# Performance work log

Measured on AMD Instinct MI355X. Metric: run time of the kernel, lower is better.

The kernel has to match this reference:

```python
import jax, jax.numpy as jnp
import numpy as np
from math import sqrt

D, H, B, L = 1024, 16, 2, 2048
DK = D // H

def linear(x, w, b):
    # torch Linear layout: w (out, in)
    return x @ w.T + b

def conv1d(x, w, b, padding, groups=1):
    # x: (B, C, L); w: (O, I/groups, K) -> torch Conv1d semantics
    y = jax.lax.conv_general_dilated(
        x, w, window_strides=(1,), padding=(padding,),
        dimension_numbers=('NCH', 'OIH', 'NCH'), feature_group_count=groups)
    return y + b[None, :, None]

def setup_inputs() -> dict:
    key = jax.random.key(0)
    ks = jax.random.split(key, 26)
    def n(k, shape, s=0.02):
        return jax.random.normal(k, shape, jnp.float32) * s
    return {
        'x': jax.random.normal(ks[0], (B, L, D), jnp.float32),
        'Wq_w': n(ks[1], (D, D)), 'Wq_b': n(ks[2], (D,)),
        'Wk_w': n(ks[3], (D, D)), 'Wk_b': n(ks[4], (D,)),
        'Wv_w': n(ks[5], (D, D)), 'Wv_b': n(ks[6], (D,)),
        'convq_w': n(ks[7], (D, D, 3)), 'convq_b': n(ks[8], (D,)),
        'convk_w': n(ks[9], (D, D, 3)), 'convk_b': n(ks[10], (D,)),
        'qproj_w': n(ks[11], (D, 2 * D)), 'qproj_b': n(ks[12], (D,)),
        'kproj_w': n(ks[13], (D, 2 * D)), 'kproj_b': n(ks[14], (D,)),
        'tau1_w': n(ks[15], (2 * D, 1, 3)), 'tau1_b': n(ks[16], (2 * D,)),
        'tau2_w': n(ks[17], (H, 2 * D, 1)), 'tau2_b': n(ks[18], (H,)),
        'del1_w': n(ks[19], (2 * D, 1, 3)), 'del1_b': n(ks[20], (2 * D,)),
        'del2_w': n(ks[21], (H, 2 * D, 1)), 'del2_b': n(ks[22], (H,)),
        'out_w': n(ks[23], (D, D)), 'out_b': n(ks[24], (D,)),
    }

def reference(x, Wq_w, Wq_b, Wk_w, Wk_b, Wv_w, Wv_b,
              convq_w, convq_b, convk_w, convk_b,
              qproj_w, qproj_b, kproj_w, kproj_b,
              tau1_w, tau1_b, tau2_w, tau2_b,
              del1_w, del1_b, del2_w, del2_b,
              out_w, out_b):
    b_, l_, _ = x.shape

    # Q branch: linear -> conv3 -> concat -> proj
    q_in = linear(x, Wq_w, Wq_b).transpose(0, 2, 1)          # (B, D, L)
    Q3 = conv1d(q_in, convq_w, convq_b, (1, 1))              # (B, D, L)
    Q_cat = jnp.concatenate([q_in, Q3], axis=1).transpose(0, 2, 1)  # (B, L, 2D)
    Q = linear(Q_cat, qproj_w, qproj_b).reshape(b_, l_, H, DK).transpose(0, 2, 1, 3)

    # K branch
    k_in = linear(x, Wk_w, Wk_b).transpose(0, 2, 1)
    K3 = conv1d(k_in, convk_w, convk_b, (1, 1))
    K_cat = jnp.concatenate([k_in, K3], axis=1).transpose(0, 2, 1)
    K = linear(K_cat, kproj_w, kproj_b).reshape(b_, l_, H, DK).transpose(0, 2, 1, 3)

    V = linear(x, Wv_w, Wv_b).reshape(b_, l_, H, DK).transpose(0, 2, 1, 3)

    # per-head tau (query-row scale) and delta (key-column bias), shape (B, H, L)
    x_conv = x.transpose(0, 2, 1)                             # (B, D, L)
    tau = jax.nn.sigmoid(conv1d(
        jax.nn.gelu(conv1d(x_conv, tau1_w, tau1_b, (1, 1), groups=D), approximate=False),
        tau2_w, tau2_b, (0, 0)))
    delta = jax.nn.sigmoid(conv1d(
        jax.nn.gelu(conv1d(x_conv, del1_w, del1_b, (1, 1), groups=D), approximate=False),
        del2_w, del2_b, (0, 0)))

    scores = jnp.einsum('bhqd,bhkd->bhqk', Q, K) / sqrt(DK)   # (B, H, L, L)
    scores = scores * tau[..., None] + delta[:, :, None, :]
    attn = jax.nn.softmax(scores, axis=-1)                    # dropout = identity (eval)
    out = jnp.einsum('bhqk,bhkd->bhqd', attn, V)
    out = out.transpose(0, 2, 1, 3).reshape(b_, l_, D)
    return linear(out, out_w, out_b)
```

## Files before the change

### kernel.cpp

```cpp
#include <hip/hip_runtime.h>

typedef __bf16 bf16_t;
typedef __bf16 bf16x8 __attribute__((ext_vector_type(8)));
typedef __bf16 bf16x4 __attribute__((ext_vector_type(4)));
typedef float f32x4 __attribute__((ext_vector_type(4)));

__device__ __forceinline__ void gload_lds16(const bf16_t* g, bf16_t* l) {
  __builtin_amdgcn_global_load_lds(
      (__attribute__((address_space(1))) void*)g,
      (__attribute__((address_space(3))) void*)l, 16, 0, 0);
}

__global__ void k_detect(const unsigned int* __restrict__ xw, int* __restrict__ flag) {
  __shared__ int red[256];
  int c = 0;
  for (int j = 0; j < 16; ++j) {
    unsigned int w = xw[threadIdx.x + (j << 8)];
    unsigned int e = (w >> 7) & 0xFF;
    c += (e >= 100 && e <= 150) ? 1 : 0;
  }
  red[threadIdx.x] = c;
  __syncthreads();
  for (int s = 128; s > 0; s >>= 1) {
    if (threadIdx.x < s) red[threadIdx.x] += red[threadIdx.x + s];
    __syncthreads();
  }
  if (threadIdx.x == 0) flag[0] = (red[0] > 2048) ? 1 : 0;
}

__device__ __constant__ long c_offs[26] = {
    0, 4194304, 4195328, 4196352, 4197376, 4198400, 4199424, 6296576,
    6297600, 8394752, 8395776, 8401920, 8403968, 8436736, 8436752,
    8442896, 8444944, 8477712, 8477728,
    0, 1048576, 2097152, 3145728,
    0, 1048576, 1049600};
struct CanonArgs { const void* src[18]; };

__global__ void k_canon(CanonArgs a, int base, int n, const int* __restrict__ flag,
                        bf16_t* __restrict__ dst) {
  long e0 = ((long)blockIdx.x * 256 + threadIdx.x) * 8;
  if (e0 >= c_offs[base + n]) return;
  int k = 0;
  while (e0 >= c_offs[base + k + 1]) ++k;
  const long rel = e0 - c_offs[base + k];
  if (flag[0]) {
    *(bf16x8*)&dst[e0] = *(const bf16x8*)((const bf16_t*)a.src[k] + rel);
  } else {
    const float* sf = (const float*)a.src[k] + rel;
    f32x4 lo = *(const f32x4*)sf;
    f32x4 hi = *(const f32x4*)(sf + 4);
    bf16x8 o;
    o[0] = (bf16_t)lo[0]; o[1] = (bf16_t)lo[1]; o[2] = (bf16_t)lo[2]; o[3] = (bf16_t)lo[3];
    o[4] = (bf16_t)hi[0]; o[5] = (bf16_t)hi[1]; o[6] = (bf16_t)hi[2]; o[7] = (bf16_t)hi[3];
    *(bf16x8*)&dst[e0] = o;
  }
}

__global__ void k_zero_pads(bf16_t* __restrict__ pad) {
  int idx = blockIdx.x * 256 + threadIdx.x;
  if (idx >= 8192) return;
  int b = idx >> 11;
  int r = (idx >> 10) & 1;
  int c = idx & 1023;
  long row = (long)b * 2050 + (r ? 2049 : 0);
  pad[row * 1024 + c] = (bf16_t)0.0f;
}

__global__ void k_convw_t2(const void* __restrict__ w0, const void* __restrict__ w1,
                           bf16_t* __restrict__ dst0, bf16_t* __restrict__ dst1,
                           const int* __restrict__ flag) {
  int idx = blockIdx.x * 256 + threadIdx.x;
  if (idx >= 6291456) return;
  const void* w = w0;
  bf16_t* dst = dst0;
  if (idx >= 3145728) { idx -= 3145728; w = w1; dst = dst1; }
  int o = idx / 3072;
  int rem = idx - o * 3072;
  int k = rem >> 10;
  int i = rem & 1023;
  int src = (o * 1024 + i) * 3 + k;
  float v = flag[0] ? (float)((const bf16_t*)w)[src] : ((const float*)w)[src];
  dst[idx] = (bf16_t)v;
}

struct GemmP {
  const bf16_t *A0, *A1;
  const bf16_t *B0, *B1, *B2;
  const bf16_t *bias0, *bias1, *bias2;
  bf16_t *C0, *C1, *C2;
  long a_jump, a1_jump;
  long cj0, cj1, cj2;
  int ksplit, lda, lda1, rpb, rpc, ldb, bsel_by_n, bshift, K, csel_by_n;
  int crs0, ccs0, crs1, ccs1, crs2, ccs2;
};

template <int BN, bool FINAL>
__global__ __launch_bounds__(256) void k_gemm(GemmP p, const int* __restrict__ flagp) {
  __shared__ __align__(16) bf16_t As[2][4096];
  __shared__ __align__(16) bf16_t Bs[2][BN * 32];
  const int tid = threadIdx.x;
  const int gx = gridDim.x;
  int lin = blockIdx.y * gx + blockIdx.x;
  const int nwg = gx * gridDim.y;
  lin = ((lin & 7) * (nwg >> 3)) + (lin >> 3);
  const int n0 = (lin % gx) * BN;
  const int m0 = (lin / gx) << 7;
  const int batch = m0 / p.rpb;
  const int cbatch = m0 / p.rpc;
  const int bidx = p.bsel_by_n ? (n0 >> 10) : (m0 >> p.bshift);
  const bf16_t* Bp = bidx == 0 ? p.B0 : (bidx == 1 ? p.B1 : p.B2);
  const bf16_t* biasp = bidx == 0 ? p.bias0 : (bidx == 1 ? p.bias1 : p.bias2);
  const long abase = (long)batch * p.a_jump;
  const long a1base = (long)cbatch * p.a1_jump;
  const int arow = tid >> 2;
  const int koff = (((tid & 3) ^ ((tid >> 3) & 3)) << 3);
  const int wid = tid >> 6, lane = tid & 63;
  const int l15 = lane & 15, lg = lane >> 4;
  const int nloc = n0 & 1023;

  constexpr int MI = (BN == 128) ? 4 : 2;
  const int wr = (BN == 128) ? ((wid >> 1) << 6) : (wid << 5);
  const int wc = (BN == 128) ? ((wid & 1) << 6) : 0;
  const int rsw = ((lg ^ (l15 >> 1)) & 3) << 3;

  f32x4 acc[MI][4];
#pragma unroll
  for (int i = 0; i < MI; ++i)
#pragma unroll
    for (int j = 0; j < 4; ++j) acc[i][j] = (f32x4){0.f, 0.f, 0.f, 0.f};

  auto stage = [&](int bufi, int k) {
    const int kg = k + koff;
#pragma unroll
    for (int half = 0; half < 2; ++half) {
      const int row = m0 + half * 64 + arow;
      const bf16_t* ap;
      if (kg < p.ksplit) ap = p.A0 + abase + (long)row * p.lda + kg;
      else               ap = p.A1 + a1base + (long)row * p.lda1 + (kg - p.ksplit);
      gload_lds16(ap, &As[bufi][half * 2048 + (tid << 3)]);
    }
    gload_lds16(Bp + (long)(nloc + arow) * p.ldb + kg, &Bs[bufi][tid << 3]);
    if (BN == 128)
      gload_lds16(Bp + (long)(nloc + 64 + arow) * p.ldb + kg, &Bs[bufi][2048 + (tid << 3)]);
  };

  const int nk = p.K >> 5;
  int buf = 0;
  stage(0, 0);
  asm volatile("s_waitcnt vmcnt(0)" ::: "memory");
  __builtin_amdgcn_s_barrier();
  __builtin_amdgcn_sched_barrier(0);
  for (int kt = 0; kt < nk; ++kt) {
    if (kt + 1 < nk) stage(buf ^ 1, (kt + 1) << 5);
    bf16x8 af[MI], bfr[4];
#pragma unroll
    for (int i = 0; i < MI; ++i)
      af[i] = *(const bf16x8*)&As[buf][((wr + (i << 4) + l15) << 5) + rsw];
#pragma unroll
    for (int j = 0; j < 4; ++j)
      bfr[j] = *(const bf16x8*)&Bs[buf][((wc + (j << 4) + l15) << 5) + rsw];
#pragma unroll
    for (int i = 0; i < MI; ++i)
#pragma unroll
      for (int j = 0; j < 4; ++j)
        acc[i][j] = __builtin_amdgcn_mfma_f32_16x16x32_bf16(af[i], bfr[j], acc[i][j], 0, 0, 0);
    if (kt + 1 < nk) asm volatile("s_waitcnt vmcnt(0)" ::: "memory");
    __builtin_amdgcn_s_barrier();
    __builtin_amdgcn_sched_barrier(0);
    buf ^= 1;
  }

  const int cp = p.csel_by_n ? (n0 >> 10) : (m0 >> p.bshift);
  bf16_t* Cb = cp == 0 ? p.C0 : (cp == 1 ? p.C1 : p.C2);
  const int crs = cp == 0 ? p.crs0 : (cp == 1 ? p.crs1 : p.crs2);
  const int ccs = cp == 0 ? p.ccs0 : (cp == 1 ? p.ccs1 : p.ccs2);
  const long cj = cp == 0 ? p.cj0 : (cp == 1 ? p.cj1 : p.cj2);
  const bool f32out = FINAL && (flagp[0] == 0);
  const long cbase = (long)batch * cj;
#pragma unroll
  for (int i = 0; i < MI; ++i) {
    const int row = m0 + wr + (i << 4) + (lg << 2);
#pragma unroll
    for (int j = 0; j < 4; ++j) {
      const int col = nloc + wc + (j << 4) + l15;
      const float bv = (float)biasp[col];
#pragma unroll
      for (int r = 0; r < 4; ++r) {
        const float val = acc[i][j][r] + bv;
        const long ci = cbase + (long)(row + r) * crs + (long)col * ccs;
        if (FINAL && f32out) ((float*)Cb)[ci] = val;
        else Cb[ci] = (bf16_t)val;
      }
    }
  }
}

__global__ __launch_bounds__(256) void k_taudelta(
    const bf16_t* __restrict__ x,
    const bf16_t* __restrict__ t1w, const bf16_t* __restrict__ t1b,
    const bf16_t* __restrict__ t2w, const bf16_t* __restrict__ t2b,
    const bf16_t* __restrict__ d1w, const bf16_t* __restrict__ d1b,
    const bf16_t* __restrict__ d2w, const bf16_t* __restrict__ d2b,
    float* __restrict__ tau, float* __restrict__ dlt)
{
  const int bt = blockIdx.x;
  const int t = bt & 2047;
  const int b = bt >> 11;
  const int tid = threadIdx.x;
  const bf16_t* xr = x + ((long)bt << 10);

  float acc[32];
#pragma unroll
  for (int i = 0; i < 32; ++i) acc[i] = 0.f;

  for (int j = 0; j < 8; ++j) {
    const int c = tid + (j << 8);
    const int src = c >> 1;
    const float x0 = (float)xr[src];
    const float xm = (t > 0) ? (float)xr[src - 1024] : 0.f;
    const float xp = (t < 2047) ? (float)xr[src + 1024] : 0.f;
    float st = (float)t1w[3 * c] * xm + (float)t1w[3 * c + 1] * x0 +
               (float)t1w[3 * c + 2] * xp + (float)t1b[c];
    float sd = (float)d1w[3 * c] * xm + (float)d1w[3 * c + 1] * x0 +
               (float)d1w[3 * c + 2] * xp + (float)d1b[c];
    const float gt = 0.5f * st * (1.f + erff(st * 0.70710678118f));
    const float gd = 0.5f * sd * (1.f + erff(sd * 0.70710678118f));
#pragma unroll
    for (int h = 0; h < 16; ++h) {
      acc[h]      += (float)t2w[(h << 11) + c] * gt;
      acc[16 + h] += (float)d2w[(h << 11) + c] * gd;
    }
  }

  __shared__ float red[256][33];
  __shared__ float red2[8][32];
#pragma unroll
  for (int i = 0; i < 32; ++i) red[tid][i] = acc[i];
  __syncthreads();
  const int i = tid & 31, g = tid >> 5;
  float p = 0.f;
#pragma unroll
  for (int k2 = 0; k2 < 32; ++k2) p += red[(g << 5) + k2][i];
  __syncthreads();
  red2[g][i] = p;
  __syncthreads();
  if (tid < 32) {
    float s = 0.f;
#pragma unroll
    for (int g2 = 0; g2 < 8; ++g2) s += red2[g2][tid];
    const int h = tid & 15;
    if (tid < 16) {
      s += (float)t2b[h];
      tau[((long)((b << 4) + h) << 11) + t] = 1.f / (1.f + __expf(-s));
    } else {
      s += (float)d2b[h];
      dlt[((long)((b << 4) + h) << 11) + t] =
          1.4426950408889634f / (1.f + __expf(-s));
    }
  }
}

__device__ __forceinline__ unsigned pk2(float a, float b) {
  union { bf16_t h[2]; unsigned u; } z;
  z.h[0] = (bf16_t)a; z.h[1] = (bf16_t)b;
  return z.u;
}

__global__ __launch_bounds__(256) void k_attn(
    const bf16_t* __restrict__ QKb, const bf16_t* __restrict__ VT,
    const float* __restrict__ tau, const float* __restrict__ dlt,
    bf16_t* __restrict__ O)
{
  const int lin = blockIdx.x;
  const int wg = ((lin & 7) << 7) + (lin >> 3);
  const int bh = wg >> 5, qt = wg & 31;
  const int tid = threadIdx.x;
  const int lane = tid & 63;
  const int wid = tid >> 6;
  const int l15 = lane & 15, lg = lane >> 4;
  const int b = bh >> 4, h = bh & 15;
  const int qbase = (qt << 6) + (wid << 4);

  const bf16_t* Qp = QKb + ((long)b << 21) + (h << 6);
  const bf16_t* Kp = QKb + 4194304 + ((long)b << 21) + (h << 6);
  const bf16_t* Vp = VT + ((long)bh << 17);
  const float* dltb = dlt + ((long)bh << 11);

  __shared__ __align__(16) bf16_t Ks[2][4096];
  __shared__ __align__(16) bf16_t Vs[2][4096];
  __shared__ unsigned Plds[4][16][32];

  bf16x8 qf[2];
#pragma unroll
  for (int kd = 0; kd < 2; ++kd)
    qf[kd] = *(const bf16x8*)&Qp[((long)(qbase + l15) << 10) + (kd << 5) + (lg << 3)];
  const float tq = tau[((long)bh << 11) + qbase + l15] * (0.125f * 1.4426950408889634f);

  bf16x8 onesf;
#pragma unroll
  for (int e = 0; e < 8; ++e) onesf[e] = (bf16_t)1.0f;

  f32x4 accO[4];
#pragma unroll
  for (int d = 0; d < 4; ++d) accO[d] = (f32x4){0.f, 0.f, 0.f, 0.f};
  f32x4 accL = (f32x4){0.f, 0.f, 0.f, 0.f};

  const int xr = (l15 & 7) << 2;

  auto stageKV = [&](int bufi, int kk) {
#pragma unroll
    for (int it = 0; it < 2; ++it) {
      const int t2 = tid + (it << 8);
      const int r = t2 >> 3, cc = (t2 & 7) ^ (r & 7);
      gload_lds16(Kp + ((long)(kk + r) << 10) + (cc << 3), &Ks[bufi][t2 << 3]);
    }
#pragma unroll
    for (int it = 0; it < 2; ++it) {
      const int t2 = tid + (it << 8);
      const int r = t2 >> 3;
      gload_lds16(Vp + ((long)r << 11) + kk + (((t2 & 7) ^ (r & 7)) << 3), &Vs[bufi][t2 << 3]);
    }
  };

  int buf = 0;
  stageKV(0, 0);
  asm volatile("s_waitcnt vmcnt(0)" ::: "memory");
  __builtin_amdgcn_s_barrier();
  __builtin_amdgcn_sched_barrier(0);

  for (int kk = 0; kk < 2048; kk += 64) {
    if (kk + 64 < 2048) stageKV(buf ^ 1, kk + 64);

    f32x4 st[4];
    __builtin_amdgcn_s_setprio(1);
#pragma unroll
    for (int kb = 0; kb < 4; ++kb) {
      f32x4 z = (f32x4){0.f, 0.f, 0.f, 0.f};
#pragma unroll
      for (int kd = 0; kd < 2; ++kd) {
        const bf16x8 kf = *(const bf16x8*)&Ks[buf][(((kb << 4) + l15) << 6) +
                                                  ((((kd << 2) | lg) ^ (l15 & 7)) << 3)];
        z = __builtin_amdgcn_mfma_f32_16x16x32_bf16(kf, qf[kd], z, 0, 0, 0);
      }
      st[kb] = z;
    }
    __builtin_amdgcn_s_setprio(0);

#pragma unroll
    for (int kb = 0; kb < 4; ++kb) {
      const f32x4 dl = *(const f32x4*)&dltb[kk + (kb << 4) + (lg << 2)];
      const float p0 = exp2f(fminf(fmaf(st[kb][0], tq, dl[0]), 30.f));
      const float p1 = exp2f(fminf(fmaf(st[kb][1], tq, dl[1]), 30.f));
      const float p2 = exp2f(fminf(fmaf(st[kb][2], tq, dl[2]), 30.f));
      const float p3 = exp2f(fminf(fmaf(st[kb][3], tq, dl[3]), 30.f));
      Plds[wid][l15][((kb << 3) + (lg << 1)) ^ xr]       = pk2(p0, p1);
      Plds[wid][l15][(((kb << 3) + (lg << 1)) | 1) ^ xr] = pk2(p2, p3);
    }
    asm volatile("s_waitcnt lgkmcnt(0)" ::: "memory");
    __builtin_amdgcn_sched_barrier(0);
    const bf16x8 pf0 = *(const bf16x8*)&Plds[wid][l15][(lg << 2) ^ xr];
    const bf16x8 pf1 = *(const bf16x8*)&Plds[wid][l15][(16 | (lg << 2)) ^ xr];
    asm volatile("s_waitcnt lgkmcnt(0)" ::: "memory");
    __builtin_amdgcn_sched_barrier(0);

    __builtin_amdgcn_s_setprio(1);
#pragma unroll
    for (int d = 0; d < 4; ++d) {
      const bf16x8 vf0 = *(const bf16x8*)&Vs[buf][(((d << 4) + l15) << 6) +
                                                 ((lg ^ (l15 & 7)) << 3)];
      const bf16x8 vf1 = *(const bf16x8*)&Vs[buf][(((d << 4) + l15) << 6) +
                                                 (((4 | lg) ^ (l15 & 7)) << 3)];
      accO[d] = __builtin_amdgcn_mfma_f32_16x16x32_bf16(vf0, pf0, accO[d], 0, 0, 0);
      accO[d] = __builtin_amdgcn_mfma_f32_16x16x32_bf16(vf1, pf1, accO[d], 0, 0, 0);
    }
    accL = __builtin_amdgcn_mfma_f32_16x16x32_bf16(onesf, pf0, accL, 0, 0, 0);
    accL = __builtin_amdgcn_mfma_f32_16x16x32_bf16(onesf, pf1, accL, 0, 0, 0);
    __builtin_amdgcn_s_setprio(0);

    if (kk + 64 < 2048) asm volatile("s_waitcnt vmcnt(0)" ::: "memory");
    __builtin_amdgcn_s_barrier();
    __builtin_amdgcn_sched_barrier(0);
    buf ^= 1;
  }

  bf16_t* Ob = O + ((long)b << 21) + (h << 6);
  const float inv = 1.f / accL[0];
#pragma unroll
  for (int d = 0; d < 4; ++d) {
    bf16x4 ov;
#pragma unroll
    for (int r = 0; r < 4; ++r) ov[r] = (bf16_t)(accO[d][r] * inv);
    *(bf16x4*)&Ob[((long)(qbase + l15) << 10) + (d << 4) + (lg << 2)] = ov;
  }
}

extern "C" void kernel_launch(void* const* d_in, const int* in_sizes, int n_in,
                              void* d_out, int out_size, void* d_ws, size_t ws_size,
                              hipStream_t stream) {
  char* w = (char*)d_ws;
  int* flag     = (int*)w;
  bf16_t* canon = (bf16_t*)(w + 16);
  bf16_t* pad   = (bf16_t*)(w + 16955472);
  bf16_t* swq   = (bf16_t*)(w + 33749072);
  bf16_t* cvout = (bf16_t*)(w + 40040528);
  bf16_t* QKb   = (bf16_t*)(w + 48429136);
  bf16_t* VT    = (bf16_t*)(w + 65206352);

  bf16_t* xc      = canon;
  bf16_t* Wq_b    = canon + 4194304;
  bf16_t* Wk_b    = canon + 4195328;
  bf16_t* Wv_b    = canon + 4196352;
  bf16_t* convq_b = canon + 4197376;
  bf16_t* convk_b = canon + 4198400;
  bf16_t* qproj_w = canon + 4199424;
  bf16_t* qproj_b = canon + 6296576;
  bf16_t* kproj_w = canon + 6297600;
  bf16_t* kproj_b = canon + 8394752;
  bf16_t* tau1_w  = canon + 8395776;
  bf16_t* tau1_b  = canon + 8401920;
  bf16_t* tau2_w  = canon + 8403968;
  bf16_t* tau2_b  = canon + 8436736;
  bf16_t* del1_w  = canon + 8436752;
  bf16_t* del1_b  = canon + 8442896;
  bf16_t* del2_w  = canon + 8444944;
  bf16_t* del2_b  = canon + 8477712;

  bf16_t* pad_q = pad;
  bf16_t* Wq_w = swq, *Wk_w = swq + 1048576, *Wv_w = swq + 2097152;
  float* tau = (float*)swq;
  float* dlt = (float*)((char*)swq + 262144);
  bf16_t* convt_q = QKb;
  bf16_t* convt_k = QKb + 4194304;
  bf16_t* cv_q = xc;
  bf16_t* cv_k = cvout;
  bf16_t* outw_bf = pad;
  bf16_t* outb_bf = pad + 1048576;
  bf16_t* attn_out = xc;

  k_detect<<<1, 256, 0, stream>>>((const unsigned int*)d_in[0], flag);

  CanonArgs ca{};
  {
    const int idxA[18] = {0, 2, 4, 6, 8, 10, 11, 12, 13, 14,
                          15, 16, 17, 18, 19, 20, 21, 22};
    for (int i = 0; i < 18; ++i) ca.src[i] = d_in[idxA[i]];
    k_canon<<<4140, 256, 0, stream>>>(ca, 0, 18, flag, canon);
  }
  {
    CanonArgs cw{};
    cw.src[0] = d_in[1]; cw.src[1] = d_in[3]; cw.src[2] = d_in[5];
    k_canon<<<1536, 256, 0, stream>>>(cw, 19, 3, flag, swq);
  }
  k_zero_pads<<<32, 256, 0, stream>>>(pad);

  {
    GemmP p{};
    p.A0 = xc; p.A1 = xc;
    p.B0 = Wq_w; p.B1 = Wk_w; p.B2 = Wv_w;
    p.bias0 = Wq_b; p.bias1 = Wk_b; p.bias2 = Wv_b;
    p.C0 = pad_q + 1024; p.C1 = pad_q + 4198400 + 1024; p.C2 = VT;
    p.a_jump = 0; p.a1_jump = 0;
    p.cj0 = 2048; p.cj1 = 2048; p.cj2 = 2095104;
    p.ksplit = 1024; p.lda = 1024; p.lda1 = 1024; p.rpb = 2048; p.rpc = 4096;
    p.ldb = 1024; p.bsel_by_n = 1; p.bshift = 12; p.K = 1024; p.csel_by_n = 1;
    p.crs0 = 1024; p.ccs0 = 1; p.crs1 = 1024; p.ccs1 = 1; p.crs2 = 1; p.ccs2 = 2048;
    k_gemm<128, false><<<dim3(24, 32), 256, 0, stream>>>(p, flag);
  }

  k_taudelta<<<4096, 256, 0, stream>>>(xc, tau1_w, tau1_b, tau2_w, tau2_b,
                                       del1_w, del1_b, del2_w, del2_b, tau, dlt);

  k_convw_t2<<<24576, 256, 0, stream>>>(d_in[7], d_in[9], convt_q, convt_k, flag);

  {
    GemmP p{};
    p.A0 = pad; p.A1 = pad;
    p.B0 = convt_q; p.B1 = convt_k; p.B2 = convt_k;
    p.bias0 = convq_b; p.bias1 = convk_b; p.bias2 = convk_b;
    p.C0 = cv_q; p.C1 = cv_k - 4194304; p.C2 = cv_k;
    p.a_jump = 2048; p.a1_jump = 0;
    p.cj0 = 0; p.cj1 = 0; p.cj2 = 0;
    p.ksplit = 3072; p.lda = 1024; p.lda1 = 1024; p.rpb = 2048; p.rpc = 4096;
    p.ldb = 3072; p.bsel_by_n = 0; p.bshift = 12; p.K = 3072; p.csel_by_n = 0;
    p.crs0 = 1024; p.ccs0 = 1; p.crs1 = 1024; p.ccs1 = 1; p.crs2 = 1024; p.ccs2 = 1;
    k_gemm<128, false><<<dim3(8, 64), 256, 0, stream>>>(p, flag);
  }

  {
    GemmP p{};
    p.A0 = pad + 1024; p.A1 = cv_q;
    p.B0 = qproj_w; p.B1 = kproj_w; p.B2 = kproj_w;
    p.bias0 = qproj_b; p.bias1 = kproj_b; p.bias2 = kproj_b;
    p.C0 = QKb; p.C1 = QKb; p.C2 = QKb;
    p.a_jump = 2048;
    p.a1_jump = 20020256 - 4194304;
    p.cj0 = 0; p.cj1 = 0; p.cj2 = 0;
    p.ksplit = 1024; p.lda = 1024; p.lda1 = 1024; p.rpb = 2048; p.rpc = 4096;
    p.ldb = 2048; p.bsel_by_n = 0; p.bshift = 12; p.K = 2048; p.csel_by_n = 0;
    p.crs0 = 1024; p.ccs0 = 1; p.crs1 = 1024; p.ccs1 = 1; p.crs2 = 1024; p.ccs2 = 1;
    k_gemm<128, false><<<dim3(8, 64), 256, 0, stream>>>(p, flag);
  }

  {
    CanonArgs co{};
    co.src[0] = d_in[23]; co.src[1] = d_in[24];
    k_canon<<<513, 256, 0, stream>>>(co, 23, 2, flag, outw_bf);
  }

  k_attn<<<1024, 256, 0, stream>>>(QKb, VT, tau, dlt, attn_out);

  {
    GemmP p{};
    p.A0 = attn_out; p.A1 = attn_out;
    p.B0 = p.B1 = p.B2 = outw_bf;
    p.bias0 = p.bias1 = p.bias2 = outb_bf;
    p.C0 = p.C1 = p.C2 = (bf16_t*)d_out;
    p.a_jump = 0; p.a1_jump = 0;
    p.cj0 = p.cj1 = p.cj2 = 0;
    p.ksplit = 1024; p.lda = 1024; p.lda1 = 1024; p.rpb = 4096; p.rpc = 4096;
    p.ldb = 1024; p.bsel_by_n = 0; p.bshift = 12; p.K = 1024; p.csel_by_n = 0;
    p.crs0 = p.crs1 = p.crs2 = 1024; p.ccs0 = p.ccs1 = p.ccs2 = 1;
    k_gemm<64, true><<<dim3(16, 32), 256, 0, stream>>>(p, flag);
  }
}
```

Baseline: 410.7 us.

## Fold conv3 weights into the projection to skip the conv GEMM

The conv1d(k=3) and the concat+projection are linear maps, so they are composed. The projection's second half is multiplied into the transposed conv weights, giving combined weights H = W2·Conv per tap. The first half of the projection is added to the centre tap, and the conv bias is folded into a bias vector. Q/K then come from a single GEMM with K=3072 over the padded linear output, which replaces the 3072-K conv GEMM plus the 2048-K projection GEMM applied to activations. This adds a weight-only GEMM, a tiled-transpose kernel for the conv weights and small add/bias kernels. It also changes rounding, since the combined weights are stored in bf16.

```diff
diff --git a/kernel.cpp b/kernel.cpp
--- a/kernel.cpp
+++ b/kernel.cpp
@@ -56,8 +56,9 @@
   }
 }
 
-__global__ void k_zero_pads(bf16_t* __restrict__ pad) {
+__global__ void k_zero_pads(bf16_t* __restrict__ pad, bf16_t* __restrict__ zvec) {
   int idx = blockIdx.x * 256 + threadIdx.x;
+  if (idx < 1024) zvec[idx] = (bf16_t)0.0f;
   if (idx >= 8192) return;
   int b = idx >> 11;
   int r = (idx >> 10) & 1;
@@ -66,31 +67,90 @@
   pad[row * 1024 + c] = (bf16_t)0.0f;
 }
 
-__global__ void k_convw_t2(const void* __restrict__ w0, const void* __restrict__ w1,
-                           bf16_t* __restrict__ dst0, bf16_t* __restrict__ dst1,
-                           const int* __restrict__ flag) {
-  int idx = blockIdx.x * 256 + threadIdx.x;
-  if (idx >= 6291456) return;
-  const void* w = w0;
-  bf16_t* dst = dst0;
-  if (idx >= 3145728) { idx -= 3145728; w = w1; dst = dst1; }
-  int o = idx / 3072;
-  int rem = idx - o * 3072;
-  int k = rem >> 10;
-  int i = rem & 1023;
-  int src = (o * 1024 + i) * 3 + k;
-  float v = flag[0] ? (float)((const bf16_t*)w)[src] : ((const float*)w)[src];
-  dst[idx] = (bf16_t)v;
+__global__ __launch_bounds__(256) void k_ctT(
+    const void* __restrict__ wq, const void* __restrict__ wk,
+    bf16_t* __restrict__ dq, bf16_t* __restrict__ dk,
+    const int* __restrict__ flag) {
+  __shared__ bf16_t T[64][72];
+  int blk = blockIdx.x;
+  const int br = blk >= 768;
+  if (br) blk -= 768;
+  const void* w = br ? wk : wq;
+  bf16_t* dst = br ? dk : dq;
+  const int ot = blk / 48, jt = blk - ot * 48;
+  const int o0 = ot << 6, j0 = jt << 6;
+  const int t = threadIdx.x;
+  const int f = flag[0];
+#pragma unroll
+  for (int it = 0; it < 2; ++it) {
+    const int ch = t + (it << 8);
+    const int r = ch >> 3, c8 = (ch & 7) << 3;
+    const long off = (long)(o0 + r) * 3072 + j0 + c8;
+    if (f) {
+      *(bf16x8*)&T[r][c8] = *(const bf16x8*)((const bf16_t*)w + off);
+    } else {
+      const float* sf = (const float*)w + off;
+      bf16x8 o8;
+#pragma unroll
+      for (int e = 0; e < 8; ++e) o8[e] = (bf16_t)sf[e];
+      *(bf16x8*)&T[r][c8] = o8;
+    }
+  }
+  __syncthreads();
+  const int j = t >> 2, oc0 = (t & 3) << 4;
+  const int jj = j0 + j;
+  const int drow = (jj % 3) * 1024 + jj / 3;
+  bf16_t* dp = dst + (long)drow * 1024 + o0 + oc0;
+#pragma unroll
+  for (int s = 0; s < 16; ++s) dp[s] = T[oc0 + s][j];
+}
+
+__global__ void k_addwp1(bf16_t* __restrict__ Hq, bf16_t* __restrict__ Hk,
+                         const bf16_t* __restrict__ qp, const bf16_t* __restrict__ kp) {
+  const long e0 = ((long)blockIdx.x * 256 + threadIdx.x) * 8;
+  if (e0 >= 2097152L) return;
+  const int br = (int)(e0 >> 20);
+  const int rem = (int)(e0 & 1048575);
+  const int o = rem >> 10, i = rem & 1023;
+  bf16_t* h = (br ? Hk : Hq) + (long)o * 3072 + 1024 + i;
+  const bf16_t* w = (br ? kp : qp) + (long)o * 2048 + i;
+  bf16x8 a = *(const bf16x8*)h;
+  bf16x8 b = *(const bf16x8*)w;
+  bf16x8 r;
+#pragma unroll
+  for (int e = 0; e < 8; ++e) r[e] = (bf16_t)((float)a[e] + (float)b[e]);
+  *(bf16x8*)h = r;
+}
+
+__global__ __launch_bounds__(256) void k_bvec(
+    const bf16_t* __restrict__ qp, const bf16_t* __restrict__ kp,
+    const bf16_t* __restrict__ cqb, const bf16_t* __restrict__ ckb,
+    const bf16_t* __restrict__ qpb, const bf16_t* __restrict__ kpb,
+    bf16_t* __restrict__ bvec) {
+  const int idx = blockIdx.x * 256 + threadIdx.x;
+  if (idx >= 2048) return;
+  const int br = idx >> 10, o = idx & 1023;
+  const bf16_t* wrow = (br ? kp : qp) + (long)o * 2048 + 1024;
+  const bf16_t* cb = br ? ckb : cqb;
+  float s = 0.f;
+  for (int m8 = 0; m8 < 1024; m8 += 8) {
+    bf16x8 w8 = *(const bf16x8*)&wrow[m8];
+    bf16x8 c8 = *(const bf16x8*)&cb[m8];
+#pragma unroll
+    for (int e = 0; e < 8; ++e) s += (float)w8[e] * (float)c8[e];
+  }
+  bvec[idx] = (bf16_t)(s + (float)((br ? kpb : qpb)[o]));
 }
 
 struct GemmP {
-  const bf16_t *A0, *A1;
+  const bf16_t *A0;
   const bf16_t *B0, *B1, *B2;
   const bf16_t *bias0, *bias1, *bias2;
   bf16_t *C0, *C1, *C2;
-  long a_jump, a1_jump;
-  long cj0, cj1, cj2;
-  int ksplit, lda, lda1, rpb, rpc, ldb, bsel_by_n, bshift, K, csel_by_n;
+  long a_jump, at_jump;
+  long cj0, cj1, cj2, ct_jump;
+  long b_jump;
+  int rpb, rpt, lda, ldb, bsel_by_n, bshift, K, csel_by_n;
   int crs0, ccs0, crs1, ccs1, crs2, ccs2;
 };
 
@@ -106,12 +166,12 @@
   const int n0 = (lin % gx) * BN;
   const int m0 = (lin / gx) << 7;
   const int batch = m0 / p.rpb;
-  const int cbatch = m0 / p.rpc;
+  const int tap = (m0 - batch * p.rpb) / p.rpt;
   const int bidx = p.bsel_by_n ? (n0 >> 10) : (m0 >> p.bshift);
-  const bf16_t* Bp = bidx == 0 ? p.B0 : (bidx == 1 ? p.B1 : p.B2);
+  const bf16_t* Bp = p.b_jump ? (p.B0 + (long)bidx * p.b_jump)
+                              : (bidx == 0 ? p.B0 : (bidx == 1 ? p.B1 : p.B2));
   const bf16_t* biasp = bidx == 0 ? p.bias0 : (bidx == 1 ? p.bias1 : p.bias2);
-  const long abase = (long)batch * p.a_jump;
-  const long a1base = (long)cbatch * p.a1_jump;
+  const long abase = (long)batch * p.a_jump + (long)tap * p.at_jump;
   const int arow = tid >> 2;
   const int koff = (((tid & 3) ^ ((tid >> 3) & 3)) << 3);
   const int wid = tid >> 6, lane = tid & 63;
@@ -134,10 +194,8 @@
 #pragma unroll
     for (int half = 0; half < 2; ++half) {
       const int row = m0 + half * 64 + arow;
-      const bf16_t* ap;
-      if (kg < p.ksplit) ap = p.A0 + abase + (long)row * p.lda + kg;
-      else               ap = p.A1 + a1base + (long)row * p.lda1 + (kg - p.ksplit);
-      gload_lds16(ap, &As[bufi][half * 2048 + (tid << 3)]);
+      gload_lds16(p.A0 + abase + (long)row * p.lda + kg,
+                  &As[bufi][half * 2048 + (tid << 3)]);
     }
     gload_lds16(Bp + (long)(nloc + arow) * p.ldb + kg, &Bs[bufi][tid << 3]);
     if (BN == 128)
@@ -176,7 +234,7 @@
   const int ccs = cp == 0 ? p.ccs0 : (cp == 1 ? p.ccs1 : p.ccs2);
   const long cj = cp == 0 ? p.cj0 : (cp == 1 ? p.cj1 : p.cj2);
   const bool f32out = FINAL && (flagp[0] == 0);
-  const long cbase = (long)batch * cj;
+  const long cbase = (long)batch * cj + (long)tap * p.ct_jump;
 #pragma unroll
   for (int i = 0; i < MI; ++i) {
     const int row = m0 + wr + (i << 4) + (lg << 2);
@@ -429,10 +487,13 @@
   bf16_t* Wq_w = swq, *Wk_w = swq + 1048576, *Wv_w = swq + 2097152;
   float* tau = (float*)swq;
   float* dlt = (float*)((char*)swq + 262144);
-  bf16_t* convt_q = QKb;
-  bf16_t* convt_k = QKb + 4194304;
-  bf16_t* cv_q = xc;
-  bf16_t* cv_k = cvout;
+  bf16_t* bvec = (bf16_t*)((char*)swq + 524288);
+  bf16_t* zvec = (bf16_t*)((char*)swq + 528384);
+  bf16_t* ctT_q = QKb;
+  bf16_t* ctT_k = QKb + 3145728;
+  bf16_t* Hq = cvout;
+  bf16_t* Hk = xc;
+  const long hk_delta = (long)(Hk - Hq);
   bf16_t* outw_bf = pad;
   bf16_t* outb_bf = pad + 1048576;
   bf16_t* attn_out = xc;
@@ -451,18 +512,19 @@
     cw.src[0] = d_in[1]; cw.src[1] = d_in[3]; cw.src[2] = d_in[5];
     k_canon<<<1536, 256, 0, stream>>>(cw, 19, 3, flag, swq);
   }
-  k_zero_pads<<<32, 256, 0, stream>>>(pad);
+  k_zero_pads<<<32, 256, 0, stream>>>(pad, zvec);
 
   {
     GemmP p{};
-    p.A0 = xc; p.A1 = xc;
+    p.A0 = xc;
     p.B0 = Wq_w; p.B1 = Wk_w; p.B2 = Wv_w;
     p.bias0 = Wq_b; p.bias1 = Wk_b; p.bias2 = Wv_b;
     p.C0 = pad_q + 1024; p.C1 = pad_q + 4198400 + 1024; p.C2 = VT;
-    p.a_jump = 0; p.a1_jump = 0;
-    p.cj0 = 2048; p.cj1 = 2048; p.cj2 = 2095104;
-    p.ksplit = 1024; p.lda = 1024; p.lda1 = 1024; p.rpb = 2048; p.rpc = 4096;
-    p.ldb = 1024; p.bsel_by_n = 1; p.bshift = 12; p.K = 1024; p.csel_by_n = 1;
+    p.a_jump = 0; p.at_jump = 0;
+    p.cj0 = 2048; p.cj1 = 2048; p.cj2 = 2095104; p.ct_jump = 0;
+    p.b_jump = 0;
+    p.rpb = 2048; p.rpt = 1 << 30; p.lda = 1024; p.ldb = 1024;
+    p.bsel_by_n = 1; p.bshift = 12; p.K = 1024; p.csel_by_n = 1;
     p.crs0 = 1024; p.ccs0 = 1; p.crs1 = 1024; p.ccs1 = 1; p.crs2 = 1; p.ccs2 = 2048;
     k_gemm<128, false><<<dim3(24, 32), 256, 0, stream>>>(p, flag);
   }
@@ -470,34 +532,41 @@
   k_taudelta<<<4096, 256, 0, stream>>>(xc, tau1_w, tau1_b, tau2_w, tau2_b,
                                        del1_w, del1_b, del2_w, del2_b, tau, dlt);
 
-  k_convw_t2<<<24576, 256, 0, stream>>>(d_in[7], d_in[9], convt_q, convt_k, flag);
+  k_ctT<<<1536, 256, 0, stream>>>(d_in[7], d_in[9], ctT_q, ctT_k, flag);
 
   {
     GemmP p{};
-    p.A0 = pad; p.A1 = pad;
-    p.B0 = convt_q; p.B1 = convt_k; p.B2 = convt_k;
-    p.bias0 = convq_b; p.bias1 = convk_b; p.bias2 = convk_b;
-    p.C0 = cv_q; p.C1 = cv_k - 4194304; p.C2 = cv_k;
-    p.a_jump = 2048; p.a1_jump = 0;
-    p.cj0 = 0; p.cj1 = 0; p.cj2 = 0;
-    p.ksplit = 3072; p.lda = 1024; p.lda1 = 1024; p.rpb = 2048; p.rpc = 4096;
-    p.ldb = 3072; p.bsel_by_n = 0; p.bshift = 12; p.K = 3072; p.csel_by_n = 0;
-    p.crs0 = 1024; p.ccs0 = 1; p.crs1 = 1024; p.ccs1 = 1; p.crs2 = 1024; p.ccs2 = 1;
-    k_gemm<128, false><<<dim3(8, 64), 256, 0, stream>>>(p, flag);
-  }
+    p.A0 = qproj_w + 1024;
+    p.B0 = ctT_q; p.B1 = ctT_q; p.B2 = ctT_q;
+    p.bias0 = p.bias1 = p.bias2 = zvec;
+    p.C0 = p.C1 = p.C2 = Hq;
+    p.a_jump = (long)(kproj_w - qproj_w) - 3072L * 2048;
+    p.at_jump = -2097152;
+    p.cj0 = p.cj1 = p.cj2 = hk_delta - 9437184;
+    p.ct_jump = -3144704;
+    p.b_jump = 1048576;
+    p.rpb = 3072; p.rpt = 1024; p.lda = 2048; p.ldb = 1024;
+    p.bsel_by_n = 0; p.bshift = 10; p.K = 1024; p.csel_by_n = 0;
+    p.crs0 = p.crs1 = p.crs2 = 3072; p.ccs0 = p.ccs1 = p.ccs2 = 1;
+    k_gemm<128, false><<<dim3(8, 48), 256, 0, stream>>>(p, flag);
+  }
+
+  k_addwp1<<<1024, 256, 0, stream>>>(Hq, Hk, qproj_w, kproj_w);
+  k_bvec<<<8, 256, 0, stream>>>(qproj_w, kproj_w, convq_b, convk_b,
+                                qproj_b, kproj_b, bvec);
 
   {
     GemmP p{};
-    p.A0 = pad + 1024; p.A1 = cv_q;
-    p.B0 = qproj_w; p.B1 = kproj_w; p.B2 = kproj_w;
-    p.bias0 = qproj_b; p.bias1 = kproj_b; p.bias2 = kproj_b;
-    p.C0 = QKb; p.C1 = QKb; p.C2 = QKb;
-    p.a_jump = 2048;
-    p.a1_jump = 20020256 - 4194304;
-    p.cj0 = 0; p.cj1 = 0; p.cj2 = 0;
-    p.ksplit = 1024; p.lda = 1024; p.lda1 = 1024; p.rpb = 2048; p.rpc = 4096;
-    p.ldb = 2048; p.bsel_by_n = 0; p.bshift = 12; p.K = 2048; p.csel_by_n = 0;
-    p.crs0 = 1024; p.ccs0 = 1; p.crs1 = 1024; p.ccs1 = 1; p.crs2 = 1024; p.ccs2 = 1;
+    p.A0 = pad;
+    p.B0 = Hq; p.B1 = Hk; p.B2 = Hk;
+    p.bias0 = bvec; p.bias1 = bvec + 1024; p.bias2 = bvec + 1024;
+    p.C0 = p.C1 = p.C2 = QKb;
+    p.a_jump = 4096; p.at_jump = 2048;
+    p.cj0 = p.cj1 = p.cj2 = 0; p.ct_jump = 0;
+    p.b_jump = 0;
+    p.rpb = 4096; p.rpt = 2048; p.lda = 1024; p.ldb = 3072;
+    p.bsel_by_n = 0; p.bshift = 12; p.K = 3072; p.csel_by_n = 0;
+    p.crs0 = p.crs1 = p.crs2 = 1024; p.ccs0 = p.ccs1 = p.ccs2 = 1;
     k_gemm<128, false><<<dim3(8, 64), 256, 0, stream>>>(p, flag);
   }
 
@@ -511,14 +580,15 @@
 
   {
     GemmP p{};
-    p.A0 = attn_out; p.A1 = attn_out;
+    p.A0 = attn_out;
     p.B0 = p.B1 = p.B2 = outw_bf;
     p.bias0 = p.bias1 = p.bias2 = outb_bf;
     p.C0 = p.C1 = p.C2 = (bf16_t*)d_out;
-    p.a_jump = 0; p.a1_jump = 0;
-    p.cj0 = p.cj1 = p.cj2 = 0;
-    p.ksplit = 1024; p.lda = 1024; p.lda1 = 1024; p.rpb = 4096; p.rpc = 4096;
-    p.ldb = 1024; p.bsel_by_n = 0; p.bshift = 12; p.K = 1024; p.csel_by_n = 0;
+    p.a_jump = 0; p.at_jump = 0;
+    p.cj0 = p.cj1 = p.cj2 = 0; p.ct_jump = 0;
+    p.b_jump = 0;
+    p.rpb = 1 << 30; p.rpt = 1 << 30; p.lda = 1024; p.ldb = 1024;
+    p.bsel_by_n = 0; p.bshift = 12; p.K = 1024; p.csel_by_n = 0;
     p.crs0 = p.crs1 = p.crs2 = 1024; p.ccs0 = p.ccs1 = p.ccs2 = 1;
     k_gemm<64, true><<<dim3(16, 32), 256, 0, stream>>>(p, flag);
   }
```

New measurement: 405.4 us. Within noise of the previous version (-1.3%).
